# Kernel tuning notes

Hardware: AMD Instinct MI355X
Metric: run time of the kernel (lower is better)

The kernel has to match this reference:

```python
import jax, jax.numpy as jnp
import numpy as np

K = 8192          # n_embeddings
D = 256           # embedding_dim
BETA = 0.25       # commitment_cost
TAU = 1.0         # gumbel-softmax temperature
B, H, W = 8, 32, 32


def setup_inputs() -> dict:
    key = jax.random.key(0)
    k1, k2, k3 = jax.random.split(key, 3)
    z_e = jax.random.normal(k1, (B, D, H, W), dtype=jnp.float32)
    # embedding init: uniform(-1/K, 1/K), matching nn.Embedding weight init in the module
    weight = jax.random.uniform(k2, (K, D), dtype=jnp.float32, minval=-1.0 / K, maxval=1.0 / K)
    # gumbel noise, one sample per (token, code) logit
    gumbel = jax.random.gumbel(k3, (B * H * W, K), dtype=jnp.float32)
    return {"z_e": z_e, "weight": weight, "gumbel": gumbel}


def reference(z_e, weight, gumbel):
    sg = jax.lax.stop_gradient
    # [B, D, H, W] -> [B, H, W, D] -> [N, D]
    z_e_p = jnp.transpose(z_e, (0, 2, 3, 1))
    flat = z_e_p.reshape(-1, D)  # [N, D]
    # squared euclidean distances to codebook: [N, K]
    distances = (jnp.sum(flat * flat, axis=1, keepdims=True)
                 + jnp.sum(weight * weight, axis=1)
                 - 2.0 * flat @ weight.T)
    logits = -distances
    # gumbel-softmax with hard straight-through one-hot
    y_soft = jax.nn.softmax((logits + gumbel) / TAU, axis=1)  # [N, K]
    encoding_indices = jnp.argmax(y_soft, axis=1)  # [N]
    y_hard = jax.nn.one_hot(encoding_indices, K, dtype=y_soft.dtype)
    soft_one_hot = sg(y_hard - y_soft) + y_soft  # hard values, soft gradient
    # quantize: one-hot matmul == gather of selected codes (kept as matmul for fidelity)
    z_q = (soft_one_hot @ weight).reshape(z_e_p.shape)  # [B, H, W, D]
    # VQ loss (codebook + commitment)
    vq_loss = (jnp.mean((z_q - sg(z_e_p)) ** 2)
               + BETA * jnp.mean((sg(z_q) - z_e_p) ** 2))
    # straight-through estimator, back to NCHW
    z_q_ste = z_e_p + sg(z_q - z_e_p)
    z_q_ste = jnp.transpose(z_q_ste, (0, 3, 1, 2))
    # perplexity of code usage
    avg_probs = jnp.mean(soft_one_hot, axis=0)
    perplexity = jnp.exp(-jnp.sum(avg_probs * jnp.log(avg_probs + 1e-10)))
    return (z_q_ste, vq_loss, perplexity, encoding_indices)
```

## Files before the change

### kernel.cpp

```cpp
#include <hip/hip_runtime.h>
#include <math.h>


typedef __attribute__((ext_vector_type(8))) short bf16x8;
typedef __attribute__((ext_vector_type(4))) float floatx4;

__device__ __forceinline__ float sq025(float q) {
  return __fmul_rn(__fmul_rn(q, q), 0.25f);
}
__device__ __forceinline__ unsigned short bf16_rne(float x) {
  unsigned int u = __float_as_uint(x);
  return (unsigned short)((u + 0x7FFFu + ((u >> 16) & 1u)) >> 16);
}
__device__ __forceinline__ float bf16f(unsigned short h) {
  return __uint_as_float(((unsigned int)h) << 16);
}
__device__ __forceinline__ void glds16(const void* g, void* l) {
  __builtin_amdgcn_global_load_lds(
      (const __attribute__((address_space(1))) unsigned int*)g,
      (__attribute__((address_space(3))) unsigned int*)l, 16, 0, 0);
}

__global__ void vq_prep_a(const float* __restrict__ z_e,
                          unsigned short* __restrict__ a_hi,
                          unsigned short* __restrict__ a_mid,
                          float* __restrict__ Arow) {
  __shared__ float tile[256][36];
  const int bx = blockIdx.x;
  const int b = bx >> 5, h = bx & 31;
  const int tid = threadIdx.x;
  const int w = tid & 31, dg = tid >> 5;
  const size_t zbase = (size_t)b * (256 * 1024) + (size_t)h * 32;
#pragma unroll 4
  for (int it = 0; it < 32; ++it) {
    const int d = dg * 32 + it;
    tile[d][w] = 2.0f * z_e[zbase + (size_t)d * 1024 + w];
  }
  __syncthreads();
  const int n0 = bx * 32;
#pragma unroll 4
  for (int w2 = 0; w2 < 32; ++w2) {
    const float q = tile[tid][w2];
    const unsigned short hh = bf16_rne(q);
    const float r1 = __fsub_rn(q, bf16f(hh));
    a_hi[(size_t)(n0 + w2) * 256 + tid] = hh;
    a_mid[(size_t)(n0 + w2) * 256 + tid] = bf16_rne(r1);
  }
  const int tg = tid >> 3, j = tid & 7;
  float halfs[2];
#pragma unroll
  for (int hf = 0; hf < 2; ++hf) {
    float r = sq025(tile[hf * 128 + j][tg]);
#pragma unroll
    for (int i = 1; i < 16; ++i)
      r = __fadd_rn(r, sq025(tile[hf * 128 + 8 * i + j][tg]));
    const float t2 = __fadd_rn(r, __shfl_xor(r, 1, 64));
    const float t4 = __fadd_rn(t2, __shfl_xor(t2, 2, 64));
    halfs[hf] = __fadd_rn(t4, __shfl_xor(t4, 4, 64));
  }
  if (j == 0) Arow[n0 + tg] = __fadd_rn(halfs[0], halfs[1]);
}

__global__ void vq_prep_w(const float* __restrict__ weight,
                          unsigned short* __restrict__ w_hi,
                          unsigned short* __restrict__ w_mid) {
  const int u = blockIdx.x * 256 + threadIdx.x;
  const float4 v = ((const float4*)weight)[u];
  float a[4] = {v.x, v.y, v.z, v.w};
  unsigned short rh[4], rm[4];
#pragma unroll
  for (int i = 0; i < 4; ++i) {
    rh[i] = bf16_rne(a[i]);
    rm[i] = bf16_rne(__fsub_rn(a[i], bf16f(rh[i])));
  }
  ushort4 oh = {rh[0], rh[1], rh[2], rh[3]};
  ushort4 om = {rm[0], rm[1], rm[2], rm[3]};
  ((ushort4*)w_hi)[u] = oh;
  ((ushort4*)w_mid)[u] = om;
}

__global__ __launch_bounds__(256, 2) void vq_score_mfma(
    const unsigned short* __restrict__ ah, const unsigned short* __restrict__ am,
    const unsigned short* __restrict__ wh, const unsigned short* __restrict__ wm,
    const float* __restrict__ gumbel, const float* __restrict__ Arow,
    float2* __restrict__ cand) {
  __shared__ unsigned short sA[2][128][32];
  __shared__ unsigned short sW[2][128][32];
  __shared__ float2 red[128][2];

  const int tid = threadIdx.x;
  const int wv = tid >> 6, lane = tid & 63;
  const int r16 = lane & 15, q = lane >> 4;
  const int wrow = (wv & 1) * 64, wcol = (wv >> 1) * 64;
  const int n0 = blockIdx.x * 128;
  const int sw = (r16 & 3) ^ ((r16 >> 2) & 1);
  const int rp = lane >> 2, pc = lane & 3;
  const int lc = pc ^ ((rp & 3) ^ ((rp >> 2) & 1));

  float Av[4][4], bv[4][4];
  int bk[4][4];
#pragma unroll
  for (int i = 0; i < 4; ++i)
#pragma unroll
    for (int rg = 0; rg < 4; ++rg) {
      Av[i][rg] = Arow[n0 + wrow + i * 16 + q * 4 + rg];
      bv[i][rg] = -3.4e38f;
      bk[i][rg] = 0x7fffffff;
    }

#pragma unroll 1
  for (int kc = 0; kc < 4; ++kc) {
    const int k0 = (blockIdx.y * 4 + kc) * 128;
    floatx4 acc[4][4];
#pragma unroll
    for (int i = 0; i < 4; ++i)
#pragma unroll
      for (int j = 0; j < 4; ++j) acc[i][j] = (floatx4){0.f, 0.f, 0.f, 0.f};

#pragma unroll 1
    for (int dc = 0; dc < 8; ++dc) {
      const int d0 = dc * 32;
      __syncthreads();
#pragma unroll
      for (int t = 0; t < 8; ++t) {
        const int gi = wv * 8 + t;
        const int m = gi >> 4, c = (gi >> 3) & 1, p = gi & 7;
        const unsigned short* gsrc = (m == 0) ? (c == 0 ? ah : am)
                                              : (c == 0 ? wh : wm);
        const int grow_ = ((m == 0) ? n0 : k0) + p * 16 + rp;
        const void* ga = gsrc + (size_t)grow_ * 256 + d0 + lc * 8;
        void* la = (m == 0) ? (void*)&sA[c][p * 16][0] : (void*)&sW[c][p * 16][0];
        glds16(ga, la);
      }
      __syncthreads();
      bf16x8 af[2][4], bf[2][4];
#pragma unroll
      for (int c = 0; c < 2; ++c)
#pragma unroll
        for (int i = 0; i < 4; ++i) {
          af[c][i] = *(const bf16x8*)&sA[c][wrow + i * 16 + r16][(q ^ sw) * 8];
          bf[c][i] = *(const bf16x8*)&sW[c][wcol + i * 16 + r16][(q ^ sw) * 8];
        }
#pragma unroll
      for (int i = 0; i < 4; ++i)
#pragma unroll
        for (int j = 0; j < 4; ++j) {
          floatx4 a = acc[i][j];
          a = __builtin_amdgcn_mfma_f32_16x16x32_bf16(af[1][i], bf[1][j], a, 0, 0, 0);
          a = __builtin_amdgcn_mfma_f32_16x16x32_bf16(af[1][i], bf[0][j], a, 0, 0, 0);
          a = __builtin_amdgcn_mfma_f32_16x16x32_bf16(af[0][i], bf[1][j], a, 0, 0, 0);
          a = __builtin_amdgcn_mfma_f32_16x16x32_bf16(af[0][i], bf[0][j], a, 0, 0, 0);
          acc[i][j] = a;
        }
    }
#pragma unroll
    for (int i = 0; i < 4; ++i)
#pragma unroll
      for (int rg = 0; rg < 4; ++rg) {
        const int nloc = wrow + i * 16 + q * 4 + rg;
        const float* grow = gumbel + (size_t)(n0 + nloc) * 8192 + k0 + wcol + r16;
#pragma unroll
        for (int j = 0; j < 4; ++j) {
          const float t2 = __fsub_rn(Av[i][rg], acc[i][j][rg]);
          const float s = __fsub_rn(grow[j * 16], t2);
          const int kk = k0 + wcol + j * 16 + r16;
          if (s > bv[i][rg]) { bv[i][rg] = s; bk[i][rg] = kk; }
        }
      }
  }
#pragma unroll
  for (int i = 0; i < 4; ++i)
#pragma unroll
    for (int rg = 0; rg < 4; ++rg) {
      float v = bv[i][rg];
      int kkk = bk[i][rg];
#pragma unroll
      for (int m = 1; m < 16; m <<= 1) {
        const float ov = __shfl_xor(v, m, 64);
        const int ok = __shfl_xor(kkk, m, 64);
        if (ov > v || (ov == v && ok < kkk)) { v = ov; kkk = ok; }
      }
      if (r16 == 0) red[wrow + i * 16 + q * 4 + rg][wv >> 1] = make_float2(v, (float)kkk);
    }
  __syncthreads();
  if (tid < 128) {
    float2 bb = red[tid][0];
    const float2 c = red[tid][1];
    if (c.x > bb.x || (c.x == bb.x && c.y < bb.y)) bb = c;
    cand[(size_t)blockIdx.y * 8192 + n0 + tid] = bb;
  }
}

__global__ void vq_reduce_cand(const float2* __restrict__ cand, int* __restrict__ idxbuf,
                               int* __restrict__ hist, float* __restrict__ out_idx) {
  const int n = blockIdx.x * 256 + threadIdx.x;
  float2 b = cand[n];
#pragma unroll
  for (int s = 1; s < 16; ++s) {
    const float2 c = cand[(size_t)s * 8192 + n];
    if (c.x > b.x || (c.x == b.x && c.y < b.y)) b = c;
  }
  const int k = (int)b.y;
  idxbuf[n] = k;
  out_idx[n] = b.y;
  atomicAdd(&hist[k], 1);
}

__global__ void vq_gather_out(const float* __restrict__ z_e, const float* __restrict__ weight,
                              const int* __restrict__ idxbuf, float* __restrict__ out0,
                              float* __restrict__ lpart) {
  __shared__ int sidx[32];
  __shared__ float sred[256];
  const int bx2 = blockIdx.x;
  const int bx = bx2 >> 1, half = bx2 & 1;
  const int b = bx >> 5, h = bx & 31;
  const int tid = threadIdx.x;
  if (tid < 32) sidx[tid] = idxbuf[bx * 32 + tid];
  __syncthreads();
  const int w = tid & 31, dg = tid >> 5;
  const int srow = sidx[w];
  const size_t base = (size_t)b * (256 * 1024) + (size_t)h * 32 + w;
  float part = 0.f;
#pragma unroll 4
  for (int it = 0; it < 16; ++it) {
    const int d = half * 128 + dg * 16 + it;
    const float qv = weight[(size_t)srow * 256 + d];
    const size_t a = base + (size_t)d * 1024;
    const float ze = z_e[a];
    const float df = qv - ze;
    out0[a] = ze + df;
    part = fmaf(df, df, part);
  }
  sred[tid] = part;
  __syncthreads();
#pragma unroll
  for (int off = 128; off > 0; off >>= 1) {
    if (tid < off) sred[tid] += sred[tid + off];
    __syncthreads();
  }
  if (tid == 0) lpart[bx2] = sred[0];
}

__global__ void vq_finalize(const float* __restrict__ lpart, const int* __restrict__ hist,
                            float* __restrict__ out) {
  __shared__ double sd[256];
  const int tid = threadIdx.x;
  sd[tid] = (double)lpart[tid] + (double)lpart[tid + 256];
  __syncthreads();
#pragma unroll
  for (int off = 128; off > 0; off >>= 1) {
    if (tid < off) sd[tid] += sd[tid + off];
    __syncthreads();
  }
  if (tid == 0) out[2097152] = (float)(1.25 * sd[0] / 2097152.0);
  __syncthreads();
  double hh = 0.0;
#pragma unroll 4
  for (int qq = 0; qq < 32; ++qq) {
    const int c = hist[tid * 32 + qq];
    const double p = (double)c / 8192.0;
    hh += p * log(p + 1e-10);
  }
  sd[tid] = hh;
  __syncthreads();
#pragma unroll
  for (int off = 128; off > 0; off >>= 1) {
    if (tid < off) sd[tid] += sd[tid + off];
    __syncthreads();
  }
  if (tid == 0) out[2097153] = (float)exp(-sd[0]);
}

extern "C" void kernel_launch(void* const* d_in, const int* in_sizes, int n_in,
                              void* d_out, int out_size, void* d_ws, size_t ws_size,
                              hipStream_t stream) {
  const float* z_e = (const float*)d_in[0];
  const float* weight = (const float*)d_in[1];
  const float* gumbel = (const float*)d_in[2];
  float* out = (float*)d_out;

  float* ws = (float*)d_ws;
  float* Arow = ws;
  int* hist = (int*)(ws + 8192);
  float* lpart = ws + 16384;
  int* idxbuf = (int*)(ws + 16896);
  float2* cand = (float2*)(ws + 25088);
  unsigned short* sb = (unsigned short*)(ws + 25088 + 262144);
  unsigned short* a_hi = sb;
  unsigned short* a_mid = sb + 2097152;
  unsigned short* w_hi = sb + 2 * 2097152;
  unsigned short* w_mid = sb + 3 * 2097152;

  hipMemsetAsync(hist, 0, 8192 * sizeof(int), stream);
  vq_prep_a<<<256, 256, 0, stream>>>(z_e, a_hi, a_mid, Arow);
  vq_prep_w<<<2048, 256, 0, stream>>>(weight, w_hi, w_mid);
  vq_score_mfma<<<dim3(64, 16), 256, 0, stream>>>(a_hi, a_mid, w_hi, w_mid,
                                                  gumbel, Arow, cand);
  vq_reduce_cand<<<32, 256, 0, stream>>>(cand, idxbuf, hist, out + 2097154);
  vq_gather_out<<<512, 256, 0, stream>>>(z_e, weight, idxbuf, out, lpart);
  vq_finalize<<<1, 256, 0, stream>>>(lpart, hist, out);
}
```

Measured before the change: 500.3 us.

## Double-buffer LDS tiles and prefetch gumbel noise in VQ score kernel

The score kernel now double-buffers the A and W LDS tiles, issuing the next d-chunk's (or next k-chunk's) global-to-LDS loads before the current chunk's MFMAs so fetches overlap compute, with one barrier per chunk instead of two. Gumbel values for the next k-chunk are preloaded into registers, and MFMA sections run at raised wave priority. The reduction scratch reuses the W buffer. LDS use doubles and the extra gumbel registers raise register pressure, which may hurt the two-blocks-per-CU occupancy target.

Result: slower. 687.6 us (+37.4%).

```diff
diff --git a/kernel.cpp b/kernel.cpp
--- a/kernel.cpp
+++ b/kernel.cpp
@@ -84,15 +84,15 @@
     const unsigned short* __restrict__ wh, const unsigned short* __restrict__ wm,
     const float* __restrict__ gumbel, const float* __restrict__ Arow,
     float2* __restrict__ cand) {
-  __shared__ unsigned short sA[2][128][32];
-  __shared__ unsigned short sW[2][128][32];
-  __shared__ float2 red[128][2];
+  __shared__ unsigned short sA[2][2][128][32];
+  __shared__ unsigned short sW[2][2][128][32];
 
   const int tid = threadIdx.x;
   const int wv = tid >> 6, lane = tid & 63;
   const int r16 = lane & 15, q = lane >> 4;
   const int wrow = (wv & 1) * 64, wcol = (wv >> 1) * 64;
   const int n0 = blockIdx.x * 128;
+  const int kbase = blockIdx.y * 512;
   const int sw = (r16 & 3) ^ ((r16 >> 2) & 1);
   const int rp = lane >> 2, pc = lane & 3;
   const int lc = pc ^ ((rp & 3) ^ ((rp >> 2) & 1));
@@ -108,39 +108,67 @@
       bk[i][rg] = 0x7fffffff;
     }
 
+  float gpre[4][4][4];
+
+  auto stage = [&](int buf, int k0s, int d0) {
+#pragma unroll
+    for (int t = 0; t < 8; ++t) {
+      const int gi = wv * 8 + t;
+      const int m = gi >> 4, c = (gi >> 3) & 1, p = gi & 7;
+      const unsigned short* gsrc = (m == 0) ? (c == 0 ? ah : am)
+                                            : (c == 0 ? wh : wm);
+      const int grow_ = ((m == 0) ? n0 : k0s) + p * 16 + rp;
+      const void* ga = gsrc + (size_t)grow_ * 256 + d0 + lc * 8;
+      void* la = (m == 0) ? (void*)&sA[buf][c][p * 16][0]
+                          : (void*)&sW[buf][c][p * 16][0];
+      glds16(ga, la);
+    }
+  };
+  auto pre_g = [&](int k0s) {
+#pragma unroll
+    for (int i = 0; i < 4; ++i)
+#pragma unroll
+      for (int rg = 0; rg < 4; ++rg) {
+        const float* grow =
+            gumbel + (size_t)(n0 + wrow + i * 16 + q * 4 + rg) * 8192 + k0s +
+            wcol + r16;
+#pragma unroll
+        for (int j = 0; j < 4; ++j) gpre[i][rg][j] = grow[j * 16];
+      }
+  };
+
+  stage(0, kbase, 0);
+  pre_g(kbase);
+  asm volatile("s_waitcnt vmcnt(0)" ::: "memory");
+  __builtin_amdgcn_s_barrier();
+  asm volatile("" ::: "memory");
+
 #pragma unroll 1
   for (int kc = 0; kc < 4; ++kc) {
-    const int k0 = (blockIdx.y * 4 + kc) * 128;
+    const int k0 = kbase + kc * 128;
     floatx4 acc[4][4];
 #pragma unroll
     for (int i = 0; i < 4; ++i)
 #pragma unroll
       for (int j = 0; j < 4; ++j) acc[i][j] = (floatx4){0.f, 0.f, 0.f, 0.f};
 
-#pragma unroll 1
+#pragma unroll
     for (int dc = 0; dc < 8; ++dc) {
-      const int d0 = dc * 32;
-      __syncthreads();
-#pragma unroll
-      for (int t = 0; t < 8; ++t) {
-        const int gi = wv * 8 + t;
-        const int m = gi >> 4, c = (gi >> 3) & 1, p = gi & 7;
-        const unsigned short* gsrc = (m == 0) ? (c == 0 ? ah : am)
-                                              : (c == 0 ? wh : wm);
-        const int grow_ = ((m == 0) ? n0 : k0) + p * 16 + rp;
-        const void* ga = gsrc + (size_t)grow_ * 256 + d0 + lc * 8;
-        void* la = (m == 0) ? (void*)&sA[c][p * 16][0] : (void*)&sW[c][p * 16][0];
-        glds16(ga, la);
+      const int buf = dc & 1;
+      if (dc < 7) {
+        stage(buf ^ 1, k0, (dc + 1) * 32);
+      } else if (kc < 3) {
+        stage(buf ^ 1, k0 + 128, 0);
       }
-      __syncthreads();
       bf16x8 af[2][4], bf[2][4];
 #pragma unroll
       for (int c = 0; c < 2; ++c)
 #pragma unroll
         for (int i = 0; i < 4; ++i) {
-          af[c][i] = *(const bf16x8*)&sA[c][wrow + i * 16 + r16][(q ^ sw) * 8];
-          bf[c][i] = *(const bf16x8*)&sW[c][wcol + i * 16 + r16][(q ^ sw) * 8];
+          af[c][i] = *(const bf16x8*)&sA[buf][c][wrow + i * 16 + r16][(q ^ sw) * 8];
+          bf[c][i] = *(const bf16x8*)&sW[buf][c][wcol + i * 16 + r16][(q ^ sw) * 8];
         }
+      __builtin_amdgcn_s_setprio(1);
 #pragma unroll
       for (int i = 0; i < 4; ++i)
 #pragma unroll
@@ -152,22 +180,28 @@
           a = __builtin_amdgcn_mfma_f32_16x16x32_bf16(af[0][i], bf[0][j], a, 0, 0, 0);
           acc[i][j] = a;
         }
+      __builtin_amdgcn_s_setprio(0);
+      asm volatile("s_waitcnt vmcnt(0)" ::: "memory");
+      __builtin_amdgcn_s_barrier();
+      asm volatile("" ::: "memory");
     }
+
 #pragma unroll
     for (int i = 0; i < 4; ++i)
 #pragma unroll
       for (int rg = 0; rg < 4; ++rg) {
-        const int nloc = wrow + i * 16 + q * 4 + rg;
-        const float* grow = gumbel + (size_t)(n0 + nloc) * 8192 + k0 + wcol + r16;
 #pragma unroll
         for (int j = 0; j < 4; ++j) {
           const float t2 = __fsub_rn(Av[i][rg], acc[i][j][rg]);
-          const float s = __fsub_rn(grow[j * 16], t2);
+          const float s = __fsub_rn(gpre[i][rg][j], t2);
           const int kk = k0 + wcol + j * 16 + r16;
           if (s > bv[i][rg]) { bv[i][rg] = s; bk[i][rg] = kk; }
         }
       }
-  }
+    if (kc < 3) pre_g(k0 + 128);
+  }
+
+  float2* redp = (float2*)&sW[0][0][0][0];
 #pragma unroll
   for (int i = 0; i < 4; ++i)
 #pragma unroll
@@ -180,12 +214,13 @@
         const int ok = __shfl_xor(kkk, m, 64);
         if (ov > v || (ov == v && ok < kkk)) { v = ov; kkk = ok; }
       }
-      if (r16 == 0) red[wrow + i * 16 + q * 4 + rg][wv >> 1] = make_float2(v, (float)kkk);
+      if (r16 == 0)
+        redp[(wrow + i * 16 + q * 4 + rg) * 2 + (wv >> 1)] = make_float2(v, (float)kkk);
     }
   __syncthreads();
   if (tid < 128) {
-    float2 bb = red[tid][0];
-    const float2 c = red[tid][1];
+    float2 bb = redp[tid * 2 + 0];
+    const float2 c = redp[tid * 2 + 1];
     if (c.x > bb.x || (c.x == bb.x && c.y < bb.y)) bb = c;
     cand[(size_t)blockIdx.y * 8192 + n0 + tid] = bb;
   }
```
